# Performance work log

Measured on AMD Instinct MI355X. Metric: run time of the kernel, lower is better.

The kernel has to match this reference:

```python
import jax, jax.numpy as jnp
import numpy as np

N, E, D = 50000, 1000000, 64
EPS = 1e-5


def setup_inputs() -> dict:
    key = jax.random.key(0)
    ks = jax.random.split(key, 20)
    inp = {
        "x": jax.random.normal(ks[0], (N, D), dtype=jnp.float32),
        "e": jax.random.uniform(ks[1], (E,), dtype=jnp.float32),
        "edge_index": jax.random.randint(ks[2], (2, E), 0, N, dtype=jnp.int64),
    }
    dims = [(3 * D, D), (D, D), (D, D), (D, D)]
    for i, (fi, fo) in enumerate(dims):
        s = 1.0 / np.sqrt(fi)
        inp[f"W{i+1}"] = jax.random.uniform(ks[3 + 4 * i], (fi, fo), minval=-s, maxval=s, dtype=jnp.float32)
        inp[f"b{i+1}"] = jax.random.uniform(ks[4 + 4 * i], (fo,), minval=-s, maxval=s, dtype=jnp.float32)
        inp[f"g{i+1}"] = jnp.ones((fo,), dtype=jnp.float32)
        inp[f"bt{i+1}"] = jnp.zeros((fo,), dtype=jnp.float32)
    return inp


def _layer(h, W, b, g, bt):
    h = h @ W + b
    mu = jnp.mean(h, axis=-1, keepdims=True)
    var = jnp.mean(jnp.square(h - mu), axis=-1, keepdims=True)
    h = (h - mu) * jax.lax.rsqrt(var + EPS) * g + bt
    return jax.nn.relu(h)


def reference(x, e, edge_index, W1, b1, g1, bt1, W2, b2, g2, bt2, W3, b3, g3, bt3, W4, b4, g4, bt4):
    start, end = edge_index[0], edge_index[1]
    we = e[:, None]  # [E,1]
    # aggregate weighted neighbor features on each side
    mi = jax.ops.segment_sum(we * x[start], end, num_segments=x.shape[0])
    mo = jax.ops.segment_sum(we * x[end], start, num_segments=x.shape[0])
    h = jnp.concatenate([mi, mo, x], axis=1)  # [N, 3D]
    h = _layer(h, W1, b1, g1, bt1)
    h = _layer(h, W2, b2, g2, bt2)
    h = _layer(h, W3, b3, g3, bt3)
    h = _layer(h, W4, b4, g4, bt4)
    return h
```

## Files before the change

kernel.cpp:

```cpp
#include <hip/hip_runtime.h>

#define NN 50000
#define NE 1000000
#define DD 64
#define EPSV 1e-5f

__global__ void detect_idx_kernel(const void* __restrict__ idx, int* __restrict__ flag,
                                  int nsample, int n_nodes) {
    const long long* p = (const long long*)idx;
    int bad = 0;
    for (int i = threadIdx.x; i < nsample; i += blockDim.x) {
        long long v = p[i];
        if (v < 0 || v >= (long long)n_nodes) bad = 1;
    }
    __shared__ int sbad;
    if (threadIdx.x == 0) sbad = 0;
    __syncthreads();
    if (bad) atomicOr(&sbad, 1);
    __syncthreads();
    if (threadIdx.x == 0) *flag = sbad ? 0 : 1;
}

__global__ __launch_bounds__(256) void scatter_kernel(
    const float* __restrict__ x, const float* __restrict__ e,
    const void* __restrict__ idx, const int* __restrict__ flag,
    float* __restrict__ mi, float* __restrict__ mo, int n_edges) {
    const int lane  = threadIdx.x & 63;
    const int slot  = (blockIdx.x * blockDim.x + threadIdx.x) >> 6;
    const int nslot = (gridDim.x * blockDim.x) >> 6;
    const bool is64 = (*flag != 0);
    const long long* p64 = (const long long*)idx;
    const int*       p32 = (const int*)idx;

    int ed = slot;
    if (ed >= n_edges) return;

    int s, t;
    if (is64) { s = (int)p64[ed]; t = (int)p64[n_edges + ed]; }
    else      { s = p32[ed];      t = p32[n_edges + ed]; }
    float w = e[ed];

    for (; ed < n_edges; ) {
        int ed2 = ed + nslot;
        int s2 = 0, t2 = 0; float w2 = 0.0f;
        if (ed2 < n_edges) {
            if (is64) { s2 = (int)p64[ed2]; t2 = (int)p64[n_edges + ed2]; }
            else      { s2 = p32[ed2];      t2 = p32[n_edges + ed2]; }
            w2 = e[ed2];
        }
        float xs = x[s * DD + lane];
        float xt = x[t * DD + lane];
        unsafeAtomicAdd(&mi[t * DD + lane], w * xs);
        unsafeAtomicAdd(&mo[s * DD + lane], w * xt);
        ed = ed2; s = s2; t = t2; w = w2;
    }
}

#define NWAVES 16
#define NPW 4

__global__ __launch_bounds__(1024, 4) void fused_mlp_kernel(
    const float* __restrict__ mi, const float* __restrict__ mo, const float* __restrict__ x,
    const float* __restrict__ W1, const float* __restrict__ b1, const float* __restrict__ g1, const float* __restrict__ bt1,
    const float* __restrict__ W2, const float* __restrict__ b2, const float* __restrict__ g2, const float* __restrict__ bt2,
    const float* __restrict__ W3, const float* __restrict__ b3, const float* __restrict__ g3, const float* __restrict__ bt3,
    const float* __restrict__ W4, const float* __restrict__ b4, const float* __restrict__ g4, const float* __restrict__ bt4,
    float* __restrict__ out, int n_nodes) {

    __shared__ float sW1[192 * 64];
    __shared__ float sW2[64 * 64];
    __shared__ float sW3[64 * 64];
    __shared__ float sW4[64 * 64];
    __shared__ float sB[4][3][64];
    __shared__ float sH[NWAVES][192 * NPW];

    const int tid = threadIdx.x;
    for (int i = tid; i < 192 * 64; i += 1024) sW1[i] = W1[i];
    for (int i = tid; i < 64 * 64; i += 1024) { sW2[i] = W2[i]; sW3[i] = W3[i]; sW4[i] = W4[i]; }
    if (tid < 64) {
        int j = tid;
        sB[0][0][j] = b1[j]; sB[0][1][j] = g1[j]; sB[0][2][j] = bt1[j];
        sB[1][0][j] = b2[j]; sB[1][1][j] = g2[j]; sB[1][2][j] = bt2[j];
        sB[2][0][j] = b3[j]; sB[2][1][j] = g3[j]; sB[2][2][j] = bt3[j];
        sB[3][0][j] = b4[j]; sB[3][1][j] = g4[j]; sB[3][2][j] = bt4[j];
    }
    __syncthreads();

    const int wid  = tid >> 6;
    const int lane = tid & 63;
    const int gw   = blockIdx.x * NWAVES + wid;
    const int nw   = gridDim.x * NWAVES;
    float4* sH4 = (float4*)&sH[wid][0];

    const int ngroups = (n_nodes + NPW - 1) / NPW;
    for (int grp = gw; grp < ngroups; grp += nw) {
        const int n0 = grp * NPW;

        float ami[NPW], amo[NPW], ax[NPW];
        #pragma unroll
        for (int m = 0; m < NPW; ++m) {
            int n = n0 + m; if (n >= n_nodes) n = n_nodes - 1;
            ami[m] = mi[n * DD + lane];
            amo[m] = mo[n * DD + lane];
            ax[m]  = x[n * DD + lane];
        }
        sH4[lane]       = make_float4(ami[0], ami[1], ami[2], ami[3]);
        sH4[64 + lane]  = make_float4(amo[0], amo[1], amo[2], amo[3]);
        sH4[128 + lane] = make_float4(ax[0], ax[1], ax[2], ax[3]);

        float acc[NPW];

        {
            float bj = sB[0][0][lane];
            #pragma unroll
            for (int m = 0; m < NPW; ++m) acc[m] = bj;
            #pragma unroll 4
            for (int k = 0; k < 192; ++k) {
                float4 hk = sH4[k];
                float  w  = sW1[k * 64 + lane];
                acc[0] = fmaf(w, hk.x, acc[0]);
                acc[1] = fmaf(w, hk.y, acc[1]);
                acc[2] = fmaf(w, hk.z, acc[2]);
                acc[3] = fmaf(w, hk.w, acc[3]);
            }
            float gj = sB[0][1][lane], btj = sB[0][2][lane];
            #pragma unroll
            for (int m = 0; m < NPW; ++m) {
                float s = acc[m];
                #pragma unroll
                for (int off = 32; off; off >>= 1) s += __shfl_xor(s, off, 64);
                float mu = s * (1.0f / 64.0f);
                float d  = acc[m] - mu;
                float s2 = d * d;
                #pragma unroll
                for (int off = 32; off; off >>= 1) s2 += __shfl_xor(s2, off, 64);
                float v = d * rsqrtf(s2 * (1.0f / 64.0f) + EPSV) * gj + btj;
                acc[m] = v > 0.0f ? v : 0.0f;
            }
            sH4[lane] = make_float4(acc[0], acc[1], acc[2], acc[3]);
        }

        const float* sWl[3] = { sW2, sW3, sW4 };
        #pragma unroll
        for (int l = 0; l < 3; ++l) {
            const float* W = sWl[l];
            float bj = sB[l + 1][0][lane];
            #pragma unroll
            for (int m = 0; m < NPW; ++m) acc[m] = bj;
            #pragma unroll 4
            for (int k = 0; k < 64; ++k) {
                float4 hk = sH4[k];
                float  w  = W[k * 64 + lane];
                acc[0] = fmaf(w, hk.x, acc[0]);
                acc[1] = fmaf(w, hk.y, acc[1]);
                acc[2] = fmaf(w, hk.z, acc[2]);
                acc[3] = fmaf(w, hk.w, acc[3]);
            }
            float gj = sB[l + 1][1][lane], btj = sB[l + 1][2][lane];
            #pragma unroll
            for (int m = 0; m < NPW; ++m) {
                float s = acc[m];
                #pragma unroll
                for (int off = 32; off; off >>= 1) s += __shfl_xor(s, off, 64);
                float mu = s * (1.0f / 64.0f);
                float d  = acc[m] - mu;
                float s2 = d * d;
                #pragma unroll
                for (int off = 32; off; off >>= 1) s2 += __shfl_xor(s2, off, 64);
                float v = d * rsqrtf(s2 * (1.0f / 64.0f) + EPSV) * gj + btj;
                acc[m] = v > 0.0f ? v : 0.0f;
            }
            if (l < 2) {
                sH4[lane] = make_float4(acc[0], acc[1], acc[2], acc[3]);
            } else {
                #pragma unroll
                for (int m = 0; m < NPW; ++m) {
                    int n = n0 + m;
                    if (n < n_nodes) out[n * DD + lane] = acc[m];
                }
            }
        }
    }
}

extern "C" void kernel_launch(void* const* d_in, const int* in_sizes, int n_in,
                              void* d_out, int out_size, void* d_ws, size_t ws_size,
                              hipStream_t stream) {
    const float* x   = (const float*)d_in[0];
    const float* e   = (const float*)d_in[1];
    const void*  idx = d_in[2];
    const float* W1 = (const float*)d_in[3],  *b1 = (const float*)d_in[4],
               * g1 = (const float*)d_in[5],  *bt1 = (const float*)d_in[6];
    const float* W2 = (const float*)d_in[7],  *b2 = (const float*)d_in[8],
               * g2 = (const float*)d_in[9],  *bt2 = (const float*)d_in[10];
    const float* W3 = (const float*)d_in[11], *b3 = (const float*)d_in[12],
               * g3 = (const float*)d_in[13], *bt3 = (const float*)d_in[14];
    const float* W4 = (const float*)d_in[15], *b4 = (const float*)d_in[16],
               * g4 = (const float*)d_in[17], *bt4 = (const float*)d_in[18];
    float* out = (float*)d_out;

    const int n_nodes = in_sizes[0] / DD;
    const int n_edges = in_sizes[1];

    float* mi = (float*)d_ws;
    float* mo = mi + (size_t)n_nodes * DD;
    int* flag = (int*)(mo + (size_t)n_nodes * DD);

    hipMemsetAsync(d_ws, 0, (size_t)2 * n_nodes * DD * sizeof(float), stream);

    detect_idx_kernel<<<1, 256, 0, stream>>>(idx, flag, 4096, n_nodes);

    scatter_kernel<<<4096, 256, 0, stream>>>(x, e, idx, flag, mi, mo, n_edges);

    fused_mlp_kernel<<<256, 1024, 0, stream>>>(
        mi, mo, x,
        W1, b1, g1, bt1, W2, b2, g2, bt2, W3, b3, g3, bt3, W4, b4, g4, bt4,
        out, n_nodes);
}
```

Baseline: 632.3 us.

## Replace atomic scatter with CSR gather and register-broadcast MLP

Builds CSR adjacency for both edge directions via histogram, scan and atomic fill, then aggregates per node with a wave-per-node gather, removing float atomics on mi/mo. The MLP kernel now keeps activations in registers, broadcasts them with readlane, stores weights transposed in padded LDS, and processes 12 nodes per wave. The gather path runs only if the workspace is large enough and adds several extra kernels plus a 2-block scan.

```diff
diff --git a/kernel.cpp b/kernel.cpp
--- a/kernel.cpp
+++ b/kernel.cpp
@@ -1,9 +1,11 @@
 #include <hip/hip_runtime.h>
 
-#define NN 50000
-#define NE 1000000
 #define DD 64
 #define EPSV 1e-5f
+
+__device__ __forceinline__ float rlane_f(float v, int k) {
+    return __int_as_float(__builtin_amdgcn_readlane(__float_as_int(v), k));
+}
 
 __global__ void detect_idx_kernel(const void* __restrict__ idx, int* __restrict__ flag,
                                   int nsample, int n_nodes) {
@@ -19,6 +21,114 @@
     if (bad) atomicOr(&sbad, 1);
     __syncthreads();
     if (threadIdx.x == 0) *flag = sbad ? 0 : 1;
+}
+
+__global__ __launch_bounds__(256) void hist_kernel(
+    const void* __restrict__ idx, const int* __restrict__ flag,
+    int* __restrict__ cnt0, int* __restrict__ cnt1, int n_edges) {
+    const bool is64 = (*flag != 0);
+    const long long* p64 = (const long long*)idx;
+    const int*       p32 = (const int*)idx;
+    int tid = blockIdx.x * blockDim.x + threadIdx.x;
+    int stride = gridDim.x * blockDim.x;
+    for (int ed = tid; ed < n_edges; ed += stride) {
+        int s, t;
+        if (is64) { s = (int)p64[ed]; t = (int)p64[n_edges + ed]; }
+        else      { s = p32[ed];      t = p32[n_edges + ed]; }
+        atomicAdd(&cnt0[t], 1);
+        atomicAdd(&cnt1[s], 1);
+    }
+}
+
+__global__ __launch_bounds__(1024) void scan_kernel(
+    const int* __restrict__ cnt0, const int* __restrict__ cnt1,
+    int* __restrict__ offs0, int* __restrict__ offs1,
+    int* __restrict__ cur0, int* __restrict__ cur1, int n) {
+    const int* cnt = blockIdx.x ? cnt1 : cnt0;
+    int* offs = blockIdx.x ? offs1 : offs0;
+    int* cur  = blockIdx.x ? cur1  : cur0;
+    const int C = (n + 1023) >> 10;
+    const int t = threadIdx.x;
+    const int base = t * C;
+    int m = n - base; if (m > C) m = C; if (m < 0) m = 0;
+
+    int sum = 0;
+    for (int i = 0; i < m; ++i) sum += cnt[base + i];
+
+    const int lane = t & 63, wid = t >> 6;
+    int s = sum;
+    #pragma unroll
+    for (int d = 1; d < 64; d <<= 1) { int u = __shfl_up(s, d, 64); if (lane >= d) s += u; }
+
+    __shared__ int wtot[16];
+    if (lane == 63) wtot[wid] = s;
+    __syncthreads();
+    if (t < 16) {
+        int w = wtot[t];
+        int sw = w;
+        #pragma unroll
+        for (int d = 1; d < 16; d <<= 1) { int u = __shfl_up(sw, d, 64); if (t >= d) sw += u; }
+        wtot[t] = sw - w;
+    }
+    __syncthreads();
+
+    int run = wtot[wid] + (s - sum);
+    for (int i = 0; i < m; ++i) {
+        offs[base + i] = run;
+        cur[base + i]  = run;
+        run += cnt[base + i];
+    }
+    if (m > 0 && base + m == n) offs[n] = run;
+}
+
+__global__ __launch_bounds__(256) void fill_kernel(
+    const void* __restrict__ idx, const float* __restrict__ e, const int* __restrict__ flag,
+    int* __restrict__ cur0, int* __restrict__ cur1,
+    int2* __restrict__ pay0, int2* __restrict__ pay1, int n_edges) {
+    const bool is64 = (*flag != 0);
+    const long long* p64 = (const long long*)idx;
+    const int*       p32 = (const int*)idx;
+    int tid = blockIdx.x * blockDim.x + threadIdx.x;
+    int stride = gridDim.x * blockDim.x;
+    for (int ed = tid; ed < n_edges; ed += stride) {
+        int s, t;
+        if (is64) { s = (int)p64[ed]; t = (int)p64[n_edges + ed]; }
+        else      { s = p32[ed];      t = p32[n_edges + ed]; }
+        int wbits = __float_as_int(e[ed]);
+        int p0 = atomicAdd(&cur0[t], 1);
+        pay0[p0] = make_int2(s, wbits);
+        int p1 = atomicAdd(&cur1[s], 1);
+        pay1[p1] = make_int2(t, wbits);
+    }
+}
+
+__global__ __launch_bounds__(256) void gather_kernel(
+    const float* __restrict__ x,
+    const int2* __restrict__ pay0, const int2* __restrict__ pay1,
+    const int* __restrict__ offs0, const int* __restrict__ offs1,
+    float* __restrict__ mi, float* __restrict__ mo, int n) {
+    const int wid = threadIdx.x >> 6, lane = threadIdx.x & 63;
+    const int gid = blockIdx.x * 4 + wid;
+    if (gid >= 2 * n) return;
+    const int dir = gid & 1, node = gid >> 1;
+    const int* offs = dir ? offs1 : offs0;
+    const int2* pay = dir ? pay1 : pay0;
+    float* dst = dir ? mo : mi;
+
+    const int o0 = offs[node], o1 = offs[node + 1];
+    float acc = 0.0f;
+    for (int b = o0; b < o1; b += 64) {
+        int2 pl = make_int2(0, 0);
+        if (b + lane < o1) pl = pay[b + lane];
+        const int cnt = min(64, o1 - b);
+        #pragma unroll 4
+        for (int j = 0; j < cnt; ++j) {
+            int src  = __builtin_amdgcn_readlane(pl.x, j);
+            float w  = __int_as_float(__builtin_amdgcn_readlane(pl.y, j));
+            acc = fmaf(w, x[src * DD + lane], acc);
+        }
+    }
+    dst[node * DD + lane] = acc;
 }
 
 __global__ __launch_bounds__(256) void scatter_kernel(
@@ -31,35 +141,53 @@
     const bool is64 = (*flag != 0);
     const long long* p64 = (const long long*)idx;
     const int*       p32 = (const int*)idx;
-
-    int ed = slot;
-    if (ed >= n_edges) return;
-
-    int s, t;
-    if (is64) { s = (int)p64[ed]; t = (int)p64[n_edges + ed]; }
-    else      { s = p32[ed];      t = p32[n_edges + ed]; }
-    float w = e[ed];
-
-    for (; ed < n_edges; ) {
-        int ed2 = ed + nslot;
-        int s2 = 0, t2 = 0; float w2 = 0.0f;
-        if (ed2 < n_edges) {
-            if (is64) { s2 = (int)p64[ed2]; t2 = (int)p64[n_edges + ed2]; }
-            else      { s2 = p32[ed2];      t2 = p32[n_edges + ed2]; }
-            w2 = e[ed2];
-        }
-        float xs = x[s * DD + lane];
-        float xt = x[t * DD + lane];
-        unsafeAtomicAdd(&mi[t * DD + lane], w * xs);
-        unsafeAtomicAdd(&mo[s * DD + lane], w * xt);
-        ed = ed2; s = s2; t = t2; w = w2;
-    }
-}
-
-#define NWAVES 16
-#define NPW 4
-
-__global__ __launch_bounds__(1024, 4) void fused_mlp_kernel(
+    for (int ed = slot; ed < n_edges; ed += nslot) {
+        int s, t;
+        if (is64) { s = (int)p64[ed]; t = (int)p64[n_edges + ed]; }
+        else      { s = p32[ed];      t = p32[n_edges + ed]; }
+        float w  = e[ed];
+        unsafeAtomicAdd(&mi[t * DD + lane], w * x[s * DD + lane]);
+        unsafeAtomicAdd(&mo[s * DD + lane], w * x[t * DD + lane]);
+    }
+}
+
+#define NPW 12
+#define MWAVES 16
+#define WT1_STRIDE 196
+#define WT_STRIDE  68
+
+template<int N>
+__device__ __forceinline__ void accum64(const float4* __restrict__ wp,
+                                        const float (&h)[N], float (&acc)[N]) {
+    #pragma unroll 2
+    for (int kb = 0; kb < 16; ++kb) {
+        float4 w4 = wp[kb];
+        int k0 = kb << 2;
+        #pragma unroll
+        for (int m = 0; m < N; ++m) acc[m] = fmaf(w4.x, rlane_f(h[m], k0), acc[m]);
+        #pragma unroll
+        for (int m = 0; m < N; ++m) acc[m] = fmaf(w4.y, rlane_f(h[m], k0 + 1), acc[m]);
+        #pragma unroll
+        for (int m = 0; m < N; ++m) acc[m] = fmaf(w4.z, rlane_f(h[m], k0 + 2), acc[m]);
+        #pragma unroll
+        for (int m = 0; m < N; ++m) acc[m] = fmaf(w4.w, rlane_f(h[m], k0 + 3), acc[m]);
+    }
+}
+
+__device__ __forceinline__ float ln_relu(float v, float g, float bt) {
+    float s = v;
+    #pragma unroll
+    for (int off = 32; off; off >>= 1) s += __shfl_xor(s, off, 64);
+    float mu = s * (1.0f / 64.0f);
+    float d = v - mu;
+    float s2 = d * d;
+    #pragma unroll
+    for (int off = 32; off; off >>= 1) s2 += __shfl_xor(s2, off, 64);
+    float r = d * rsqrtf(s2 * (1.0f / 64.0f) + EPSV) * g + bt;
+    return fmaxf(r, 0.0f);
+}
+
+__global__ __launch_bounds__(1024) void fused_mlp2(
     const float* __restrict__ mi, const float* __restrict__ mo, const float* __restrict__ x,
     const float* __restrict__ W1, const float* __restrict__ b1, const float* __restrict__ g1, const float* __restrict__ bt1,
     const float* __restrict__ W2, const float* __restrict__ b2, const float* __restrict__ g2, const float* __restrict__ bt2,
@@ -67,16 +195,23 @@
     const float* __restrict__ W4, const float* __restrict__ b4, const float* __restrict__ g4, const float* __restrict__ bt4,
     float* __restrict__ out, int n_nodes) {
 
-    __shared__ float sW1[192 * 64];
-    __shared__ float sW2[64 * 64];
-    __shared__ float sW3[64 * 64];
-    __shared__ float sW4[64 * 64];
+    __shared__ float sWT1[64 * WT1_STRIDE];
+    __shared__ float sWT2[64 * WT_STRIDE];
+    __shared__ float sWT3[64 * WT_STRIDE];
+    __shared__ float sWT4[64 * WT_STRIDE];
     __shared__ float sB[4][3][64];
-    __shared__ float sH[NWAVES][192 * NPW];
 
     const int tid = threadIdx.x;
-    for (int i = tid; i < 192 * 64; i += 1024) sW1[i] = W1[i];
-    for (int i = tid; i < 64 * 64; i += 1024) { sW2[i] = W2[i]; sW3[i] = W3[i]; sW4[i] = W4[i]; }
+    for (int i = tid; i < 192 * 64; i += 1024) {
+        int k = i >> 6, j = i & 63;
+        sWT1[j * WT1_STRIDE + k] = W1[i];
+    }
+    for (int i = tid; i < 64 * 64; i += 1024) {
+        int k = i >> 6, j = i & 63;
+        sWT2[j * WT_STRIDE + k] = W2[i];
+        sWT3[j * WT_STRIDE + k] = W3[i];
+        sWT4[j * WT_STRIDE + k] = W4[i];
+    }
     if (tid < 64) {
         int j = tid;
         sB[0][0][j] = b1[j]; sB[0][1][j] = g1[j]; sB[0][2][j] = bt1[j];
@@ -86,99 +221,57 @@
     }
     __syncthreads();
 
-    const int wid  = tid >> 6;
-    const int lane = tid & 63;
-    const int gw   = blockIdx.x * NWAVES + wid;
-    const int nw   = gridDim.x * NWAVES;
-    float4* sH4 = (float4*)&sH[wid][0];
+    const int wid = tid >> 6, lane = tid & 63;
+    const int gw = blockIdx.x * MWAVES + wid;
+    const int nw = gridDim.x * MWAVES;
+    const float4* wt1 = (const float4*)&sWT1[lane * WT1_STRIDE];
+    const float4* wt2 = (const float4*)&sWT2[lane * WT_STRIDE];
+    const float4* wt3 = (const float4*)&sWT3[lane * WT_STRIDE];
+    const float4* wt4 = (const float4*)&sWT4[lane * WT_STRIDE];
 
     const int ngroups = (n_nodes + NPW - 1) / NPW;
     for (int grp = gw; grp < ngroups; grp += nw) {
         const int n0 = grp * NPW;
 
-        float ami[NPW], amo[NPW], ax[NPW];
+        float hmi[NPW], hmo[NPW], hx[NPW];
         #pragma unroll
         for (int m = 0; m < NPW; ++m) {
             int n = n0 + m; if (n >= n_nodes) n = n_nodes - 1;
-            ami[m] = mi[n * DD + lane];
-            amo[m] = mo[n * DD + lane];
-            ax[m]  = x[n * DD + lane];
-        }
-        sH4[lane]       = make_float4(ami[0], ami[1], ami[2], ami[3]);
-        sH4[64 + lane]  = make_float4(amo[0], amo[1], amo[2], amo[3]);
-        sH4[128 + lane] = make_float4(ax[0], ax[1], ax[2], ax[3]);
-
-        float acc[NPW];
+            hmi[m] = mi[n * DD + lane];
+            hmo[m] = mo[n * DD + lane];
+            hx[m]  = x[n * DD + lane];
+        }
+
+        float acc[NPW], h[NPW];
 
         {
             float bj = sB[0][0][lane];
             #pragma unroll
             for (int m = 0; m < NPW; ++m) acc[m] = bj;
-            #pragma unroll 4
-            for (int k = 0; k < 192; ++k) {
-                float4 hk = sH4[k];
-                float  w  = sW1[k * 64 + lane];
-                acc[0] = fmaf(w, hk.x, acc[0]);
-                acc[1] = fmaf(w, hk.y, acc[1]);
-                acc[2] = fmaf(w, hk.z, acc[2]);
-                acc[3] = fmaf(w, hk.w, acc[3]);
-            }
+            accum64(wt1 +  0, hmi, acc);
+            accum64(wt1 + 16, hmo, acc);
+            accum64(wt1 + 32, hx,  acc);
             float gj = sB[0][1][lane], btj = sB[0][2][lane];
             #pragma unroll
-            for (int m = 0; m < NPW; ++m) {
-                float s = acc[m];
-                #pragma unroll
-                for (int off = 32; off; off >>= 1) s += __shfl_xor(s, off, 64);
-                float mu = s * (1.0f / 64.0f);
-                float d  = acc[m] - mu;
-                float s2 = d * d;
-                #pragma unroll
-                for (int off = 32; off; off >>= 1) s2 += __shfl_xor(s2, off, 64);
-                float v = d * rsqrtf(s2 * (1.0f / 64.0f) + EPSV) * gj + btj;
-                acc[m] = v > 0.0f ? v : 0.0f;
-            }
-            sH4[lane] = make_float4(acc[0], acc[1], acc[2], acc[3]);
-        }
-
-        const float* sWl[3] = { sW2, sW3, sW4 };
+            for (int m = 0; m < NPW; ++m) h[m] = ln_relu(acc[m], gj, btj);
+        }
+
+        const float4* wts[3] = { wt2, wt3, wt4 };
         #pragma unroll
         for (int l = 0; l < 3; ++l) {
-            const float* W = sWl[l];
             float bj = sB[l + 1][0][lane];
             #pragma unroll
             for (int m = 0; m < NPW; ++m) acc[m] = bj;
-            #pragma unroll 4
-            for (int k = 0; k < 64; ++k) {
-                float4 hk = sH4[k];
-                float  w  = W[k * 64 + lane];
-                acc[0] = fmaf(w, hk.x, acc[0]);
-                acc[1] = fmaf(w, hk.y, acc[1]);
-                acc[2] = fmaf(w, hk.z, acc[2]);
-                acc[3] = fmaf(w, hk.w, acc[3]);
-            }
+            accum64(wts[l], h, acc);
             float gj = sB[l + 1][1][lane], btj = sB[l + 1][2][lane];
             #pragma unroll
-            for (int m = 0; m < NPW; ++m) {
-                float s = acc[m];
-                #pragma unroll
-                for (int off = 32; off; off >>= 1) s += __shfl_xor(s, off, 64);
-                float mu = s * (1.0f / 64.0f);
-                float d  = acc[m] - mu;
-                float s2 = d * d;
-                #pragma unroll
-                for (int off = 32; off; off >>= 1) s2 += __shfl_xor(s2, off, 64);
-                float v = d * rsqrtf(s2 * (1.0f / 64.0f) + EPSV) * gj + btj;
-                acc[m] = v > 0.0f ? v : 0.0f;
-            }
-            if (l < 2) {
-                sH4[lane] = make_float4(acc[0], acc[1], acc[2], acc[3]);
-            } else {
-                #pragma unroll
-                for (int m = 0; m < NPW; ++m) {
-                    int n = n0 + m;
-                    if (n < n_nodes) out[n * DD + lane] = acc[m];
-                }
-            }
+            for (int m = 0; m < NPW; ++m) h[m] = ln_relu(acc[m], gj, btj);
+        }
+
+        #pragma unroll
+        for (int m = 0; m < NPW; ++m) {
+            int n = n0 + m;
+            if (n < n_nodes) out[n * DD + lane] = h[m];
         }
     }
 }
@@ -204,15 +297,33 @@
 
     float* mi = (float*)d_ws;
     float* mo = mi + (size_t)n_nodes * DD;
-    int* flag = (int*)(mo + (size_t)n_nodes * DD);
-
-    hipMemsetAsync(d_ws, 0, (size_t)2 * n_nodes * DD * sizeof(float), stream);
+    int*  flag = (int*)(mo + (size_t)n_nodes * DD);
+    char* p = (char*)(flag + 2);
+    int2* pay0 = (int2*)p;            p += (size_t)n_edges * sizeof(int2);
+    int2* pay1 = (int2*)p;            p += (size_t)n_edges * sizeof(int2);
+    int* cnt0  = (int*)p;             p += (size_t)n_nodes * 4;
+    int* cnt1  = (int*)p;             p += (size_t)n_nodes * 4;
+    int* offs0 = (int*)p;             p += (size_t)(n_nodes + 1) * 4;
+    int* offs1 = (int*)p;             p += (size_t)(n_nodes + 1) * 4;
+    int* cur0  = (int*)p;             p += (size_t)n_nodes * 4;
+    int* cur1  = (int*)p;             p += (size_t)n_nodes * 4;
+    const size_t need = (size_t)(p - (char*)d_ws);
 
     detect_idx_kernel<<<1, 256, 0, stream>>>(idx, flag, 4096, n_nodes);
 
-    scatter_kernel<<<4096, 256, 0, stream>>>(x, e, idx, flag, mi, mo, n_edges);
-
-    fused_mlp_kernel<<<256, 1024, 0, stream>>>(
+    if (ws_size >= need) {
+        hipMemsetAsync(cnt0, 0, (size_t)2 * n_nodes * 4, stream);
+        hist_kernel<<<2048, 256, 0, stream>>>(idx, flag, cnt0, cnt1, n_edges);
+        scan_kernel<<<2, 1024, 0, stream>>>(cnt0, cnt1, offs0, offs1, cur0, cur1, n_nodes);
+        fill_kernel<<<2048, 256, 0, stream>>>(idx, e, flag, cur0, cur1, pay0, pay1, n_edges);
+        const int nblocks = (2 * n_nodes + 3) / 4;
+        gather_kernel<<<nblocks, 256, 0, stream>>>(x, pay0, pay1, offs0, offs1, mi, mo, n_nodes);
+    } else {
+        hipMemsetAsync(d_ws, 0, (size_t)2 * n_nodes * DD * sizeof(float), stream);
+        scatter_kernel<<<4096, 256, 0, stream>>>(x, e, idx, flag, mi, mo, n_edges);
+    }
+
+    fused_mlp2<<<256, 1024, 0, stream>>>(
         mi, mo, x,
         W1, b1, g1, bt1, W2, b2, g2, bt2, W3, b3, g3, bt3, W4, b4, g4, bt4,
         out, n_nodes);
```

Measured after the change: 774.7 us. +22.5%, slower.
